# Kernel tuning notes

Hardware: AMD Instinct MI355X
Metric: run time of the kernel (lower is better)

## Reference

```python
import jax, jax.numpy as jnp
import numpy as np

PERIOD = 25
ADJUST = True
ALPHA = 2.0 / (PERIOD + 1.0)


def setup_inputs() -> dict:
    key = jax.random.key(0)
    x = jax.random.normal(key, (32, 4096, 256), dtype=jnp.float32)
    return {"x": x}


def reference(x):
    # x: (B, T, F). Faithful to the keras layer: EMA_0 = x_0;
    # for t>=1: e_t = (alpha*x_t + (1-alpha)*e_{t-1}) / max(1-(1-alpha)^(t+1), 1e-10)
    # (the bias-corrected value is fed back into the recurrence, matching the source).
    B, T, F = x.shape
    alpha = jnp.asarray(ALPHA, x.dtype)
    oma = jnp.asarray(1.0 - ALPHA, x.dtype)

    if ADJUST:
        t = jnp.arange(1, T, dtype=x.dtype)  # t = 1..T-1
        w = jnp.maximum(1.0 - oma ** (t + 1.0), jnp.asarray(1e-10, x.dtype))  # (T-1,)
    else:
        w = jnp.ones((T - 1,), dtype=x.dtype)

    e0 = x[:, 0, :]                      # (B, F)
    xs = jnp.swapaxes(x[:, 1:, :], 0, 1)  # (T-1, B, F), time-major for scan

    def step(e_prev, inp):
        x_t, w_t = inp
        e = (alpha * x_t + oma * e_prev) / w_t
        return e, e

    _, es = jax.lax.scan(step, e0, (xs, w))  # es: (T-1, B, F)
    ema = jnp.concatenate([e0[:, None, :], jnp.swapaxes(es, 0, 1)], axis=1)
    return ema
```

## Files before the change

kernel.cpp:

```cpp
#include <hip/hip_runtime.h>


namespace {

constexpr int kT = 4096;
constexpr int kF4 = 64;
constexpr int kL = 512;
constexpr int kHalo = 256;
constexpr int kNC = kT / kL;
constexpr int kG = 16;

constexpr double kAlphaD = 2.0 / 26.0;
constexpr float kAlpha = (float)kAlphaD;
constexpr float kOma   = (float)(1.0 - kAlphaD);

__device__ __forceinline__ void load_group(const float4* __restrict__ p,
                                           float4 (&buf)[kG]) {
#pragma unroll
  for (int i = 0; i < kG; ++i) buf[i] = p[i * kF4];
}

__device__ __forceinline__ void store_group(float4* __restrict__ p,
                                            const float4 (&buf)[kG]) {
#pragma unroll
  for (int i = 0; i < kG; ++i) p[i * kF4] = buf[i];
}

__device__ __forceinline__ void step_fast(float4& e, const float4 v) {
  e.x = fmaf(kOma, e.x, kAlpha * v.x);
  e.y = fmaf(kOma, e.y, kAlpha * v.y);
  e.z = fmaf(kOma, e.z, kAlpha * v.z);
  e.w = fmaf(kOma, e.w, kAlpha * v.w);
}

__device__ __forceinline__ void group_fast(float4 (&buf)[kG], float4& e) {
#pragma unroll
  for (int i = 0; i < kG; ++i) {
    step_fast(e, buf[i]);
    buf[i] = e;
  }
}

}

__global__ __launch_bounds__(64, 1) void ema_kernel(const float* __restrict__ x,
                                                    float* __restrict__ out) {
  const int blk = blockIdx.x;
  const int c = blk & (kNC - 1);
  const int b = blk / kNC;
  const int lane = threadIdx.x;

  const float4* xb = reinterpret_cast<const float4*>(x) + (size_t)b * kT * kF4 + lane;
  float4* ob = reinterpret_cast<float4*>(out) + (size_t)b * kT * kF4 + lane;

  float4 e = make_float4(0.f, 0.f, 0.f, 0.f);
  float4 bufA[kG], bufB[kG];

  if (c == 0) {
    const float4* px = xb;
    float4* po = ob;
    double p = (double)kOma;
    constexpr int NGrp = kL / kG;

    load_group(px, bufA);
    px += kG * kF4;
    for (int g = 0; g < NGrp; g += 2) {
      load_group(px, bufB);
      px += kG * kF4;
      {
        const int tbase = g * kG;
#pragma unroll
        for (int i = 0; i < kG; ++i) {
          const float4 v = bufA[i];
          if (tbase + i == 0) {
            e = v;
          } else {
            p *= (double)kOma;
            const float w = fmaxf(1.0f - (float)p, 1e-10f);
            const float inv = 1.0f / w;
            step_fast(e, v);
            e.x *= inv; e.y *= inv; e.z *= inv; e.w *= inv;
          }
          bufA[i] = e;
        }
      }
      store_group(po, bufA);
      po += kG * kF4;
      if (g + 2 < NGrp) {
        load_group(px, bufA);
        px += kG * kF4;
      }
      {
#pragma unroll
        for (int i = 0; i < kG; ++i) {
          const float4 v = bufB[i];
          p *= (double)kOma;
          const float w = fmaxf(1.0f - (float)p, 1e-10f);
          const float inv = 1.0f / w;
          step_fast(e, v);
          e.x *= inv; e.y *= inv; e.z *= inv; e.w *= inv;
          bufB[i] = e;
        }
      }
      store_group(po, bufB);
      po += kG * kF4;
    }
  } else {
    const float4* px = xb + (size_t)(c * kL - kHalo) * kF4;
    float4* po = ob + (size_t)(c * kL) * kF4;
    constexpr int NGrp = (kHalo + kL) / kG;
    constexpr int HGrp = kHalo / kG;

    load_group(px, bufA);
    px += kG * kF4;
    for (int g = 0; g < NGrp; g += 2) {
      load_group(px, bufB);
      px += kG * kF4;
      group_fast(bufA, e);
      if (g >= HGrp) {
        store_group(po, bufA);
        po += kG * kF4;
      }
      if (g + 2 < NGrp) {
        load_group(px, bufA);
        px += kG * kF4;
      }
      group_fast(bufB, e);
      if (g + 1 >= HGrp) {
        store_group(po, bufB);
        po += kG * kF4;
      }
    }
  }
}

extern "C" void kernel_launch(void* const* d_in, const int* in_sizes, int n_in,
                              void* d_out, int out_size, void* d_ws, size_t ws_size,
                              hipStream_t stream) {
  (void)in_sizes; (void)n_in; (void)d_ws; (void)ws_size; (void)out_size;
  const float* x = reinterpret_cast<const float*>(d_in[0]);
  float* out = reinterpret_cast<float*>(d_out);
  constexpr int kBatches = 32;
  dim3 grid(kBatches * kNC);
  dim3 block(64);
  hipLaunchKernelGGL(ema_kernel, grid, block, 0, stream, x, out);
}
```

Before: 245.3 us.

## Shrink time chunks and halo to launch many more blocks per batch

Splits each batch's time axis into 64-step chunks with a 128-step warm-up halo, raising the block count eightfold, and swizzles block order. The first few chunks run an exact bias-corrected path starting from a pow-computed decay factor; the rest use the uncorrected recurrence. The aim is to fill the GPU instead of running one wavefront per CU, at the cost of tripling redundant input reads and a shorter halo that leaves a larger truncation error.

```diff
diff --git a/kernel.cpp b/kernel.cpp
--- a/kernel.cpp
+++ b/kernel.cpp
@@ -1,14 +1,17 @@
 #include <hip/hip_runtime.h>
+#include <math.h>
 
 
 namespace {
 
 constexpr int kT = 4096;
 constexpr int kF4 = 64;
-constexpr int kL = 512;
-constexpr int kHalo = 256;
+constexpr int kL = 64;
+constexpr int kHalo = 128;
 constexpr int kNC = kT / kL;
 constexpr int kG = 16;
+constexpr int kBatches = 32;
+constexpr int kBlocks = kBatches * kNC;
 
 constexpr double kAlphaD = 2.0 / 26.0;
 constexpr float kAlpha = (float)kAlphaD;
@@ -33,104 +36,86 @@
   e.w = fmaf(kOma, e.w, kAlpha * v.w);
 }
 
-__device__ __forceinline__ void group_fast(float4 (&buf)[kG], float4& e) {
+template <bool EXACT>
+__device__ __forceinline__ void process_group(float4 (&buf)[kG], float4& e,
+                                              double& p, int tbase) {
 #pragma unroll
   for (int i = 0; i < kG; ++i) {
-    step_fast(e, buf[i]);
+    const float4 v = buf[i];
+    if (EXACT) {
+      if (tbase + i == 0) {
+        e = v;
+      } else {
+        p *= (double)kOma;
+        const float w = fmaxf(1.0f - (float)p, 1e-10f);
+        const float inv = 1.0f / w;
+        step_fast(e, v);
+        e.x *= inv; e.y *= inv; e.z *= inv; e.w *= inv;
+      }
+    } else {
+      step_fast(e, v);
+    }
     buf[i] = e;
+  }
+}
+
+template <bool EXACT>
+__device__ __forceinline__ void run_chunk(const float4* __restrict__ px,
+                                          float4* __restrict__ po,
+                                          int ng, int hg, int t0) {
+  float4 e = make_float4(0.f, 0.f, 0.f, 0.f);
+  float4 bufA[kG], bufB[kG];
+  double p = 0.0;
+  if (EXACT) {
+    p = pow((double)kOma, (double)t0);
+    if (t0 == 0) p = 1.0;
+  }
+  if (EXACT) p = pow((double)kOma, (double)(t0 == 0 ? 1 : t0));
+
+  load_group(px, bufA);
+  px += kG * kF4;
+  for (int g = 0; g < ng; g += 2) {
+    load_group(px, bufB);
+    px += kG * kF4;
+    process_group<EXACT>(bufA, e, p, t0 + g * kG);
+    if (g >= hg) {
+      store_group(po, bufA);
+      po += kG * kF4;
+    }
+    if (g + 2 < ng) {
+      load_group(px, bufA);
+      px += kG * kF4;
+    }
+    process_group<EXACT>(bufB, e, p, t0 + (g + 1) * kG);
+    if (g + 1 >= hg) {
+      store_group(po, bufB);
+      po += kG * kF4;
+    }
   }
 }
 
 }
 
-__global__ __launch_bounds__(64, 1) void ema_kernel(const float* __restrict__ x,
+__global__ __launch_bounds__(64, 2) void ema_kernel(const float* __restrict__ x,
                                                     float* __restrict__ out) {
-  const int blk = blockIdx.x;
-  const int c = blk & (kNC - 1);
-  const int b = blk / kNC;
-  const int lane = threadIdx.x;
+  const int sw = (blockIdx.x & 7) * (kBlocks / 8) + (blockIdx.x >> 3);
+  const int b = sw / kNC;
+  const int c = sw & (kNC - 1);
 
-  const float4* xb = reinterpret_cast<const float4*>(x) + (size_t)b * kT * kF4 + lane;
-  float4* ob = reinterpret_cast<float4*>(out) + (size_t)b * kT * kF4 + lane;
+  const int t0 = (c >= 2) ? (c * kL - kHalo) : 0;
+  const int rows = (c == 0) ? kL : (c == 1 ? 2 * kL : kHalo + kL);
+  const int ng = rows / kG;
+  const int hg = (c * kL - t0) / kG;
 
-  float4 e = make_float4(0.f, 0.f, 0.f, 0.f);
-  float4 bufA[kG], bufB[kG];
+  const float4* px = reinterpret_cast<const float4*>(x) +
+                     ((size_t)b * kT + t0) * kF4 + threadIdx.x;
+  float4* po = reinterpret_cast<float4*>(out) +
+               ((size_t)b * kT + (size_t)c * kL) * kF4 + threadIdx.x;
 
-  if (c == 0) {
-    const float4* px = xb;
-    float4* po = ob;
-    double p = (double)kOma;
-    constexpr int NGrp = kL / kG;
-
-    load_group(px, bufA);
-    px += kG * kF4;
-    for (int g = 0; g < NGrp; g += 2) {
-      load_group(px, bufB);
-      px += kG * kF4;
-      {
-        const int tbase = g * kG;
-#pragma unroll
-        for (int i = 0; i < kG; ++i) {
-          const float4 v = bufA[i];
-          if (tbase + i == 0) {
-            e = v;
-          } else {
-            p *= (double)kOma;
-            const float w = fmaxf(1.0f - (float)p, 1e-10f);
-            const float inv = 1.0f / w;
-            step_fast(e, v);
-            e.x *= inv; e.y *= inv; e.z *= inv; e.w *= inv;
-          }
-          bufA[i] = e;
-        }
-      }
-      store_group(po, bufA);
-      po += kG * kF4;
-      if (g + 2 < NGrp) {
-        load_group(px, bufA);
-        px += kG * kF4;
-      }
-      {
-#pragma unroll
-        for (int i = 0; i < kG; ++i) {
-          const float4 v = bufB[i];
-          p *= (double)kOma;
-          const float w = fmaxf(1.0f - (float)p, 1e-10f);
-          const float inv = 1.0f / w;
-          step_fast(e, v);
-          e.x *= inv; e.y *= inv; e.z *= inv; e.w *= inv;
-          bufB[i] = e;
-        }
-      }
-      store_group(po, bufB);
-      po += kG * kF4;
-    }
+  if (c < 6) {
+    run_chunk<true>(px, po, ng, hg, t0);
   } else {
-    const float4* px = xb + (size_t)(c * kL - kHalo) * kF4;
-    float4* po = ob + (size_t)(c * kL) * kF4;
-    constexpr int NGrp = (kHalo + kL) / kG;
-    constexpr int HGrp = kHalo / kG;
-
-    load_group(px, bufA);
-    px += kG * kF4;
-    for (int g = 0; g < NGrp; g += 2) {
-      load_group(px, bufB);
-      px += kG * kF4;
-      group_fast(bufA, e);
-      if (g >= HGrp) {
-        store_group(po, bufA);
-        po += kG * kF4;
-      }
-      if (g + 2 < NGrp) {
-        load_group(px, bufA);
-        px += kG * kF4;
-      }
-      group_fast(bufB, e);
-      if (g + 1 >= HGrp) {
-        store_group(po, bufB);
-        po += kG * kF4;
-      }
-    }
+    run_chunk<false>(px, po, ng, hg, t0);
   }
 }
 
@@ -140,8 +125,5 @@
   (void)in_sizes; (void)n_in; (void)d_ws; (void)ws_size; (void)out_size;
   const float* x = reinterpret_cast<const float*>(d_in[0]);
   float* out = reinterpret_cast<float*>(d_out);
-  constexpr int kBatches = 32;
-  dim3 grid(kBatches * kNC);
-  dim3 block(64);
-  hipLaunchKernelGGL(ema_kernel, grid, block, 0, stream, x, out);
+  hipLaunchKernelGGL(ema_kernel, dim3(kBlocks), dim3(64), 0, stream, x, out);
 }
```

Result: slower. 257.2 us (+4.8%).
